# Optimization experiments

Hardware: AMD Instinct MI355X
Metric: run time of the kernel (lower is better)

## Reference

```python
import jax, jax.numpy as jnp
import numpy as np

B, O, D = 256, 128, 128          # batch, out_features (positions), per-position feat
IN = O * D                        # flattened in_features = 16384
NEG = -9.0e15                     # matches torch's -9e15 mask value


def setup_inputs() -> dict:
    key = jax.random.key(0)
    k1, k2 = jax.random.split(key, 2)
    enc = jax.random.normal(k1, (B, O, D), jnp.float32)
    W = jax.random.normal(k2, (O, IN), jnp.float32) / np.float32(np.sqrt(IN))
    b = jnp.zeros((O,), jnp.float32)
    return {"enc": enc, "W": W, "b": b}


def _step(enc, mask, W, b, k_count, key):
    """One decode step: linear -> error probe -> masked log-softmax -> sample.
    enc: [B,O,D], mask: [B,O] (1 = still available). k_count = #already-masked per row."""
    p = enc.reshape(B, IN) @ W.T + b                       # [B,O] raw scores
    order = jnp.argsort(-p, axis=1)                        # descending argsort of RAW p
    top_idx = jnp.take(order, k_count, axis=1)             # [B] (k_count+1)-th largest
    err = (jnp.take_along_axis(mask, top_idx[:, None], 1)[:, 0] == 0).astype(jnp.int32)
    pm = jnp.where(mask == 0, NEG, p)
    logp = jax.nn.log_softmax(pm, axis=1)                  # [B,O]
    pos = jax.random.categorical(key, logp)                # multinomial(exp(logp), 1)
    ls = jnp.take_along_axis(logp, pos[:, None], 1)[:, 0]  # chosen log-prob [B]
    new_mask = mask - jax.nn.one_hot(pos, O, dtype=mask.dtype)
    return pos, ls, err, new_mask


def reference(enc, W, b):
    mask0 = jnp.ones((B, O), jnp.float32)
    keys = jax.random.split(jax.random.key(42), O)
    # step 0: no enc masking, all-ones mask (k_count = 0)
    pos0, ls0, err0, mask = _step(enc, mask0, W, b, 0, keys[0])

    def body(carry, xs):
        enc_c, mask = carry
        j, key = xs
        enc_c = enc_c * mask[:, :, None]                   # zero out chosen positions
        pos, ls, err, mask = _step(enc_c, mask, W, b, j, key)
        return (enc_c, mask), (pos, ls, err)

    (_, _), (poss, lss, errs) = jax.lax.scan(
        body, (enc, mask), (jnp.arange(1, O), keys[1:]))
    # original prepends each new position: column 0 = last step sampled
    positions = jnp.flip(jnp.concatenate([pos0[None], poss], axis=0), axis=0).T  # [B,O]
    log_softmaxs = ls0 + lss.sum(axis=0)                   # [B]
    errors = err0 + errs.sum(axis=0)                       # [B] int32
    return positions, log_softmaxs, errors
```

## Files before the change

### kernel.cpp

```cpp
#include <hip/hip_runtime.h>
#include <stdint.h>

#define B_   256
#define O_   128
#define D_   128
#define IN_  16384
#define NEGF (-9.0e15f)
#define TINYF 1.1754943508222875e-38f

__device__ __forceinline__ void tf2x32(uint32_t k0, uint32_t k1,
                                       uint32_t x0, uint32_t x1,
                                       uint32_t* o0, uint32_t* o1) {
  uint32_t k2 = k0 ^ k1 ^ 0x1BD11BDAu;
#define TFR(r) { x0 += x1; x1 = (x1 << (r)) | (x1 >> (32 - (r))); x1 ^= x0; }
  x0 += k0; x1 += k1;
  TFR(13) TFR(15) TFR(26) TFR(6)
  x0 += k1; x1 += k2 + 1u;
  TFR(17) TFR(29) TFR(16) TFR(24)
  x0 += k2; x1 += k0 + 2u;
  TFR(13) TFR(15) TFR(26) TFR(6)
  x0 += k0; x1 += k1 + 3u;
  TFR(17) TFR(29) TFR(16) TFR(24)
  x0 += k1; x1 += k2 + 4u;
  TFR(13) TFR(15) TFR(26) TFR(6)
  x0 += k2; x1 += k0 + 5u;
#undef TFR
  *o0 = x0; *o1 = x1;
}

__device__ __forceinline__ float gumbel_bits(uint32_t bits) {
  float f = __uint_as_float((bits >> 9) | 0x3f800000u) - 1.0f;
  float u = fmaxf(TINYF, f + TINYF);
  return -logf(-logf(u));
}

__device__ __forceinline__ uint32_t mono32(float x) {
  int b = __float_as_int(x);
  return (uint32_t)b ^ ((uint32_t)(b >> 31) | 0x80000000u);
}

__device__ __forceinline__ float rl_f(float v, int l) {
  return __int_as_float(__builtin_amdgcn_readlane(__float_as_int(v), l));
}

#define DPPF(x, ctrl) __int_as_float(__builtin_amdgcn_mov_dpp( \
    __float_as_int(x), (ctrl), 0xf, 0xf, true))

__device__ __forceinline__ float wredmaxf(float x) {
  x = fmaxf(x, DPPF(x, 0xB1));
  x = fmaxf(x, DPPF(x, 0x4E));
  x = fmaxf(x, DPPF(x, 0x141));
  x = fmaxf(x, DPPF(x, 0x140));
  x = fmaxf(x, DPPF(x, 0x142));
  x = fmaxf(x, DPPF(x, 0x143));
  return rl_f(x, 63);
}
__device__ __forceinline__ float wredsumf(float x) {
  x = x + DPPF(x, 0xB1);
  x = x + DPPF(x, 0x4E);
  x = x + DPPF(x, 0x141);
  x = x + DPPF(x, 0x140);
  x = x + DPPF(x, 0x142);
  x = x + DPPF(x, 0x143);
  return rl_f(x, 63);
}

__global__ __launch_bounds__(256, 2) void build_M(
    const float* __restrict__ enc, const float* __restrict__ W,
    float* __restrict__ M) {
  const int p   = blockIdx.x;
  const int og0 = (blockIdx.y & 1) * 64;
  const int b0  = (blockIdx.y >> 1) * 128;
  const int t   = threadIdx.x;

  __shared__ float Ws[64 * 132];

  {
    const int rgrp = t >> 5;
    const int c16  = t & 31;
#pragma unroll
    for (int k = 0; k < 8; k++) {
      int row = k * 8 + rgrp;
      *(float4*)(Ws + row * 132 + c16 * 4) =
          *(const float4*)(W + (size_t)(og0 + row) * IN_ + p * D_ + c16 * 4);
    }
  }

  const int og = t & 15;
  const int bg = t >> 4;

  const float* eb = enc + ((size_t)(b0 + bg) * O_ + p) * D_;
  const size_t bstride = (size_t)16 * O_ * D_;

  float4 ev[8], evn[8];
#pragma unroll
  for (int bi = 0; bi < 8; bi++)
    ev[bi] = *(const float4*)(eb + bi * bstride);

  __syncthreads();

  float acc0[8][4] = {}, acc1[8][4] = {};

  for (int dc = 0; dc < 128; dc += 4) {
    if (dc < 124) {
#pragma unroll
      for (int bi = 0; bi < 8; bi++)
        evn[bi] = *(const float4*)(eb + bi * bstride + dc + 4);
    }
    float4 wv[4];
#pragma unroll
    for (int oi = 0; oi < 4; oi++)
      wv[oi] = *(const float4*)(Ws + (og + 16 * oi) * 132 + dc);
#pragma unroll
    for (int bi = 0; bi < 8; bi++)
#pragma unroll
      for (int oi = 0; oi < 4; oi++) {
        acc0[bi][oi] += ev[bi].x * wv[oi].x;
        acc1[bi][oi] += ev[bi].y * wv[oi].y;
        acc0[bi][oi] += ev[bi].z * wv[oi].z;
        acc1[bi][oi] += ev[bi].w * wv[oi].w;
      }
#pragma unroll
    for (int bi = 0; bi < 8; bi++) ev[bi] = evn[bi];
  }

#pragma unroll
  for (int bi = 0; bi < 8; bi++) {
    int b = b0 + bg + 16 * bi;
#pragma unroll
    for (int oi = 0; oi < 4; oi++) {
      int o = og0 + og + 16 * oi;
      M[((size_t)b * O_ + p) * O_ + o] = acc0[bi][oi] + acc1[bi][oi];
    }
  }
}

__global__ __launch_bounds__(512, 1) void sampler(
    const float* __restrict__ M, const float* __restrict__ bias,
    const float* __restrict__ enc, const float* __restrict__ W, int use_M,
    float* __restrict__ out_pos, float* __restrict__ out_ls,
    float* __restrict__ out_err) {
  const int b = blockIdx.x;
  const int t = threadIdx.x;
  const int lane = t & 63;
  const int w = t >> 6;

  __shared__ float  Mlds[O_ * O_];
  __shared__ float  Glds[O_ * O_];
  __shared__ double snapPd[16 * 64 * 2];
  __shared__ unsigned long long snapMk[16 * 2];
  __shared__ double lsSlot[16];
  __shared__ int    errSlot[16];
  __shared__ int    posb[O_];
  __shared__ int    flagG[16];
  __shared__ int    chainRel[16];
  __shared__ int    stageDone;

  volatile int* vFlagG = flagG;
  volatile int* vRel   = chainRel;
  volatile int* vSD    = &stageDone;

  const float b1f = bias[lane], b2f = bias[lane + 64];

  if (t < 16) { flagG[t] = 0; chainRel[t] = 0; }
  if (t == 16) stageDone = 0;
  __syncthreads();

  if (!use_M) {
    for (int idx = t; idx < O_ * O_; idx += 512) {
      int p = idx >> 7, o = idx & 127;
      const float* er = enc + ((size_t)b * O_ + p) * D_;
      const float* wr = W + (size_t)o * IN_ + p * D_;
      float s = 0.f;
      for (int d = 0; d < D_; d += 4) {
        float4 e4 = *(const float4*)(er + d);
        float4 w4 = *(const float4*)(wr + d);
        s += e4.x * w4.x + e4.y * w4.y + e4.z * w4.z + e4.w * w4.w;
      }
      Mlds[p * O_ + ((o & 63) << 1) + (o >> 6)] = s;
    }
    __syncthreads();
    if (t == 0) *vSD = 4;
  } else if (w < 4) {
    const float* Mb = M + (size_t)b * O_ * O_;
    for (int p = w * 32; p < w * 32 + 32; p++) {
      float v1 = Mb[p * O_ + lane];
      float v2 = Mb[p * O_ + 64 + lane];
      float2 mv; mv.x = v1; mv.y = v2;
      *(float2*)&Mlds[p * O_ + 2 * lane] = mv;
    }
    __threadfence_block();
    if (lane == 0) atomicAdd(&stageDone, 1);
  }

  if (w >= 4) {
#pragma unroll 1
    for (int k = 0; k < 4; k++) {
      int c = (w - 4) + 4 * k;
      for (int r = 8 * c; r < 8 * c + 8; r++) {
        uint32_t k0j, k1j, w0, w1;
        tf2x32(0u, 42u, 0u, (uint32_t)r, &k0j, &k1j);
        uint32_t m1 = (uint32_t)(b * O_ + lane);
        tf2x32(k0j, k1j, 0u, m1, &w0, &w1);
        float g1 = gumbel_bits(w0 ^ w1);
        tf2x32(k0j, k1j, 0u, m1 + 64u, &w0, &w1);
        float g2 = gumbel_bits(w0 ^ w1);
        float2 gv; gv.x = g1; gv.y = g2;
        *(float2*)&Glds[r * O_ + 2 * lane] = gv;
      }
      __threadfence_block();
      if (lane == 0) vFlagG[c] = 1;
    }
  }

  if (w == 0) {
    __builtin_amdgcn_s_setprio(3);
    while (*vSD < 4) __builtin_amdgcn_s_sleep(1);
    __threadfence_block();

    double Pd1 = 0.0, Pd2 = 0.0;
    for (int p = 0; p < O_; p++) {
      float2 mv = *(float2*)&Mlds[p * O_ + 2 * lane];
      Pd1 += (double)mv.x;
      Pd2 += (double)mv.y;
    }

    int mk1 = 0, mk2 = 0;
    unsigned long long bmk1 = 0ull, bmk2 = 0ull;
    while (vFlagG[0] == 0) __builtin_amdgcn_s_sleep(1);
    __threadfence_block();
    float2 gcur = *(float2*)&Glds[2 * lane];

    for (int j = 0; j < O_; j++) {
      if ((j & 7) == 0) {
        int c = j >> 3;
        if (c < 15) {
          while (vFlagG[c + 1] == 0) __builtin_amdgcn_s_sleep(1);
          __threadfence_block();
        }
        double2 pv; pv.x = Pd1; pv.y = Pd2;
        *(double2*)&snapPd[(c * 64 + lane) * 2] = pv;
        if (lane == 0) { snapMk[c * 2] = bmk1; snapMk[c * 2 + 1] = bmk2; }
      }
      float pm1 = mk1 ? NEGF : ((float)Pd1 + b1f);
      float pm2 = mk2 ? NEGF : ((float)Pd2 + b2f);
      float2 gnext;
      if (j < O_ - 1) gnext = *(float2*)&Glds[(j + 1) * O_ + 2 * lane];

      float z1 = pm1 + gcur.x, z2 = pm2 + gcur.y;
      float m = fmaxf(z1, z2);
      m = fmaxf(m, DPPF(m, 0xB1));
      m = fmaxf(m, DPPF(m, 0x4E));
      m = fmaxf(m, DPPF(m, 0x141));
      m = fmaxf(m, DPPF(m, 0x140));
      m = fmaxf(m, DPPF(m, 0x142));
      m = fmaxf(m, DPPF(m, 0x143));
      float zm = rl_f(m, 63);
      float thr = zm - 1e-2f;
      unsigned long long n1 = __ballot(z1 > thr);
      unsigned long long n2 = __ballot(z2 > thr);

      int pos;
      if (__popcll(n1) + __popcll(n2) == 1) {
        pos = n1 ? (__ffsll(n1) - 1) : (64 + __ffsll(n2) - 1);
      } else {
        float mx = wredmaxf(fmaxf(pm1, pm2));
        float s1 = pm1 - mx, s2 = pm2 - mx;
        float ss = wredsumf(expf(s1) + expf(s2));
        float lse = logf(ss);
        float y1 = (s1 - lse) + gcur.x;
        float y2 = (s2 - lse) + gcur.y;
        float ym = wredmaxf(fmaxf(y1, y2));
        unsigned long long c1 = __ballot(y1 == ym);
        unsigned long long c2 = __ballot(y2 == ym);
        pos = c1 ? (__ffsll(c1) - 1) : (64 + __ffsll(c2) - 1);
      }

      if (lane == 0) posb[j] = pos;
      mk1 |= (lane == pos);
      mk2 |= (lane + 64 == pos);
      if (pos < 64) bmk1 |= 1ull << pos; else bmk2 |= 1ull << (pos - 64);
      float2 mv = *(float2*)&Mlds[pos * O_ + 2 * lane];
      Pd1 -= (double)mv.x;
      Pd2 -= (double)mv.y;
      if ((j & 7) == 7) {
        __threadfence_block();
        if (lane == 0) vRel[j >> 3] = 1;
      }
      gcur = gnext;
    }
    out_pos[(size_t)b * O_ + lane]      = (float)posb[127 - lane];
    out_pos[(size_t)b * O_ + 64 + lane] = (float)posb[63 - lane];
  }

  if (w >= 1) {
    for (int c = w - 1; c < 16; c += 7) {
      while (vRel[c] == 0) __builtin_amdgcn_s_sleep(1);
      __threadfence_block();
      double2 pv = *(double2*)&snapPd[(c * 64 + lane) * 2];
      double P1 = pv.x, P2 = pv.y;
      unsigned long long bmk1 = snapMk[c * 2], bmk2 = snapMk[c * 2 + 1];
      double ls_acc = 0.0;
      int err_acc = 0;
      for (int j = 8 * c; j < 8 * c + 8; j++) {
        float p1 = (float)P1 + b1f;
        float p2 = (float)P2 + b2f;
        uint64_t K1 = ((uint64_t)mono32(p1) << 7) | (uint32_t)(127 - lane);
        uint64_t K2 = ((uint64_t)mono32(p2) << 7) | (uint32_t)(63 - lane);
        uint64_t P = 0;
#pragma unroll
        for (int bit = 38; bit >= 0; --bit) {
          uint64_t cand = P | (1ull << bit);
          int c1 = __popcll(__ballot(K1 >= cand));
          int c2 = __popcll(__ballot(K2 >= cand));
          if (c1 + c2 > j) P = cand;
        }
        unsigned long long t1 = __ballot(K1 == P), t2 = __ballot(K2 == P);
        int topl, msk;
        if (t1) { topl = __ffsll(t1) - 1; msk = (int)((bmk1 >> topl) & 1); }
        else    { topl = __ffsll(t2) - 1; msk = (int)((bmk2 >> topl) & 1); }
        err_acc += msk;

        float pm1 = ((bmk1 >> lane) & 1) ? NEGF : p1;
        float pm2 = ((bmk2 >> lane) & 1) ? NEGF : p2;
        float mx = wredmaxf(fmaxf(pm1, pm2));
        float ss = wredsumf(expf(pm1 - mx) + expf(pm2 - mx));
        float lse = logf(ss);
        int pos = posb[j];
        float psel = rl_f((pos < 64) ? p1 : p2, pos & 63);
        ls_acc += (double)((psel - mx) - lse);

        if (pos < 64) bmk1 |= 1ull << pos; else bmk2 |= 1ull << (pos - 64);
        float2 mv = *(float2*)&Mlds[pos * O_ + 2 * lane];
        P1 -= (double)mv.x;
        P2 -= (double)mv.y;
      }
      if (lane == 0) { lsSlot[c] = ls_acc; errSlot[c] = err_acc; }
    }
  }
  __syncthreads();

  if (t == 0) {
    double lt = 0.0; int et = 0;
    for (int i = 0; i < 16; i++) { lt += lsSlot[i]; et += errSlot[i]; }
    out_ls[b]  = (float)lt;
    out_err[b] = (float)et;
  }
}

extern "C" void kernel_launch(void* const* d_in, const int* in_sizes, int n_in,
                              void* d_out, int out_size, void* d_ws, size_t ws_size,
                              hipStream_t stream) {
  const float* enc  = (const float*)d_in[0];
  const float* W    = (const float*)d_in[1];
  const float* bias = (const float*)d_in[2];
  float* out     = (float*)d_out;
  float* out_pos = out;
  float* out_ls  = out + B_ * O_;
  float* out_err = out + B_ * O_ + B_;

  float* M = (float*)d_ws;
  const size_t needM = (size_t)B_ * O_ * O_ * sizeof(float);
  int use_M = (ws_size >= needM) ? 1 : 0;

  if (use_M) build_M<<<dim3(O_, 4), 256, 0, stream>>>(enc, W, M);
  sampler<<<dim3(B_), 512, 0, stream>>>(M, bias, enc, W, use_M,
                                        out_pos, out_ls, out_err);
}
```

Before: 150.7 us.

## Rebalance sampler warps: parallel column sums, shared key cache, split tail chunk

The column-sum prefix that wave 0 used to compute serially over all 128 rows is now split across waves 1-4 as partial double sums, and wave 0 only adds four partials. The per-row Threefry key derivation is computed once into shared memory, and Gumbel generation is spread over more waves, with waves 1-4 handling the later chunks. The final 8-step scoring chunk is split into two 4-step chunks so the tail work after the serial chain finishes is shorter. Bias plus Gumbel is also precomputed one step ahead to shorten the serial critical path. The cost is extra shared memory and more complex flag and chunk bookkeeping. Changing the order of the double summation can also change rounding slightly.

```diff
diff --git a/kernel.cpp b/kernel.cpp
--- a/kernel.cpp
+++ b/kernel.cpp
@@ -147,14 +147,16 @@
 
   __shared__ float  Mlds[O_ * O_];
   __shared__ float  Glds[O_ * O_];
-  __shared__ double snapPd[16 * 64 * 2];
-  __shared__ unsigned long long snapMk[16 * 2];
-  __shared__ double lsSlot[16];
-  __shared__ int    errSlot[16];
+  __shared__ double snapPd[17 * 64 * 2];
+  __shared__ unsigned long long snapMk[17 * 2];
+  __shared__ double lsSlot[17];
+  __shared__ int    errSlot[17];
   __shared__ int    posb[O_];
   __shared__ int    flagG[16];
-  __shared__ int    chainRel[16];
+  __shared__ int    chainRel[17];
   __shared__ int    stageDone;
+  __shared__ double partPd[4][64][2];
+  __shared__ uint32_t Klds[O_ * 2];
 
   volatile int* vFlagG = flagG;
   volatile int* vRel   = chainRel;
@@ -162,8 +164,13 @@
 
   const float b1f = bias[lane], b2f = bias[lane + 64];
 
-  if (t < 16) { flagG[t] = 0; chainRel[t] = 0; }
-  if (t == 16) stageDone = 0;
+  if (t < O_) {
+    uint32_t a, bb;
+    tf2x32(0u, 42u, 0u, (uint32_t)t, &a, &bb);
+    Klds[2 * t] = a; Klds[2 * t + 1] = bb;
+  }
+  if (t < 17) { chainRel[t] = 0; if (t < 16) flagG[t] = 0; }
+  if (t == 17) stageDone = 0;
   __syncthreads();
 
   if (!use_M) {
@@ -180,26 +187,41 @@
       Mlds[p * O_ + ((o & 63) << 1) + (o >> 6)] = s;
     }
     __syncthreads();
-    if (t == 0) *vSD = 4;
-  } else if (w < 4) {
+    if (w >= 1 && w <= 4) {
+      int q = w - 1;
+      double P1 = 0.0, P2 = 0.0;
+      for (int p = 32 * q; p < 32 * q + 32; p++) {
+        float2 mv = *(float2*)&Mlds[p * O_ + 2 * lane];
+        P1 += (double)mv.x;
+        P2 += (double)mv.y;
+      }
+      partPd[q][lane][0] = P1; partPd[q][lane][1] = P2;
+      __threadfence_block();
+      if (lane == 0) atomicAdd(&stageDone, 1);
+    }
+  } else if (w >= 1 && w <= 4) {
+    int q = w - 1;
     const float* Mb = M + (size_t)b * O_ * O_;
-    for (int p = w * 32; p < w * 32 + 32; p++) {
+    double P1 = 0.0, P2 = 0.0;
+    for (int p = 32 * q; p < 32 * q + 32; p++) {
       float v1 = Mb[p * O_ + lane];
       float v2 = Mb[p * O_ + 64 + lane];
       float2 mv; mv.x = v1; mv.y = v2;
       *(float2*)&Mlds[p * O_ + 2 * lane] = mv;
-    }
+      P1 += (double)v1;
+      P2 += (double)v2;
+    }
+    partPd[q][lane][0] = P1; partPd[q][lane][1] = P2;
     __threadfence_block();
     if (lane == 0) atomicAdd(&stageDone, 1);
   }
 
-  if (w >= 4) {
+  if (w >= 5) {
 #pragma unroll 1
-    for (int k = 0; k < 4; k++) {
-      int c = (w - 4) + 4 * k;
+    for (int c = w - 5; c < 8; c += 3) {
       for (int r = 8 * c; r < 8 * c + 8; r++) {
-        uint32_t k0j, k1j, w0, w1;
-        tf2x32(0u, 42u, 0u, (uint32_t)r, &k0j, &k1j);
+        uint32_t k0j = Klds[2 * r], k1j = Klds[2 * r + 1];
+        uint32_t w0, w1;
         uint32_t m1 = (uint32_t)(b * O_ + lane);
         tf2x32(k0j, k1j, 0u, m1, &w0, &w1);
         float g1 = gumbel_bits(w0 ^ w1);
@@ -211,6 +233,23 @@
       __threadfence_block();
       if (lane == 0) vFlagG[c] = 1;
     }
+  } else if (w >= 1) {
+#pragma unroll 1
+    for (int c = 7 + w; c < 16; c += 4) {
+      for (int r = 8 * c; r < 8 * c + 8; r++) {
+        uint32_t k0j = Klds[2 * r], k1j = Klds[2 * r + 1];
+        uint32_t w0, w1;
+        uint32_t m1 = (uint32_t)(b * O_ + lane);
+        tf2x32(k0j, k1j, 0u, m1, &w0, &w1);
+        float g1 = gumbel_bits(w0 ^ w1);
+        tf2x32(k0j, k1j, 0u, m1 + 64u, &w0, &w1);
+        float g2 = gumbel_bits(w0 ^ w1);
+        float2 gv; gv.x = g1; gv.y = g2;
+        *(float2*)&Glds[r * O_ + 2 * lane] = gv;
+      }
+      __threadfence_block();
+      if (lane == 0) vFlagG[c] = 1;
+    }
   }
 
   if (w == 0) {
@@ -218,36 +257,36 @@
     while (*vSD < 4) __builtin_amdgcn_s_sleep(1);
     __threadfence_block();
 
-    double Pd1 = 0.0, Pd2 = 0.0;
-    for (int p = 0; p < O_; p++) {
-      float2 mv = *(float2*)&Mlds[p * O_ + 2 * lane];
-      Pd1 += (double)mv.x;
-      Pd2 += (double)mv.y;
-    }
+    double Pd1 = ((partPd[0][lane][0] + partPd[1][lane][0]) +
+                  partPd[2][lane][0]) + partPd[3][lane][0];
+    double Pd2 = ((partPd[0][lane][1] + partPd[1][lane][1]) +
+                  partPd[2][lane][1]) + partPd[3][lane][1];
 
     int mk1 = 0, mk2 = 0;
     unsigned long long bmk1 = 0ull, bmk2 = 0ull;
     while (vFlagG[0] == 0) __builtin_amdgcn_s_sleep(1);
     __threadfence_block();
     float2 gcur = *(float2*)&Glds[2 * lane];
+    float bz1 = b1f + gcur.x, bz2 = b2f + gcur.y;
 
     for (int j = 0; j < O_; j++) {
-      if ((j & 7) == 0) {
+      if ((j & 7) == 0 || j == 124) {
         int c = j >> 3;
-        if (c < 15) {
+        if ((j & 7) == 0 && c < 15) {
           while (vFlagG[c + 1] == 0) __builtin_amdgcn_s_sleep(1);
           __threadfence_block();
         }
+        int sc = (j < 124) ? (j >> 3) : 16;
         double2 pv; pv.x = Pd1; pv.y = Pd2;
-        *(double2*)&snapPd[(c * 64 + lane) * 2] = pv;
-        if (lane == 0) { snapMk[c * 2] = bmk1; snapMk[c * 2 + 1] = bmk2; }
-      }
-      float pm1 = mk1 ? NEGF : ((float)Pd1 + b1f);
-      float pm2 = mk2 ? NEGF : ((float)Pd2 + b2f);
+        *(double2*)&snapPd[(sc * 64 + lane) * 2] = pv;
+        if (lane == 0) { snapMk[sc * 2] = bmk1; snapMk[sc * 2 + 1] = bmk2; }
+      }
+      float pmf1 = (float)Pd1, pmf2 = (float)Pd2;
+      float z1 = mk1 ? NEGF : (pmf1 + bz1);
+      float z2 = mk2 ? NEGF : (pmf2 + bz2);
       float2 gnext;
       if (j < O_ - 1) gnext = *(float2*)&Glds[(j + 1) * O_ + 2 * lane];
 
-      float z1 = pm1 + gcur.x, z2 = pm2 + gcur.y;
       float m = fmaxf(z1, z2);
       m = fmaxf(m, DPPF(m, 0xB1));
       m = fmaxf(m, DPPF(m, 0x4E));
@@ -264,6 +303,8 @@
       if (__popcll(n1) + __popcll(n2) == 1) {
         pos = n1 ? (__ffsll(n1) - 1) : (64 + __ffsll(n2) - 1);
       } else {
+        float pm1 = mk1 ? NEGF : (pmf1 + b1f);
+        float pm2 = mk2 ? NEGF : (pmf2 + b2f);
         float mx = wredmaxf(fmaxf(pm1, pm2));
         float s1 = pm1 - mx, s2 = pm2 - mx;
         float ss = wredsumf(expf(s1) + expf(s2));
@@ -283,18 +324,18 @@
       float2 mv = *(float2*)&Mlds[pos * O_ + 2 * lane];
       Pd1 -= (double)mv.x;
       Pd2 -= (double)mv.y;
-      if ((j & 7) == 7) {
-        __threadfence_block();
-        if (lane == 0) vRel[j >> 3] = 1;
-      }
+      if (j == 123) { __threadfence_block(); if (lane == 0) vRel[15] = 1; }
+      else if (j == 127) { __threadfence_block(); if (lane == 0) vRel[16] = 1; }
+      else if ((j & 7) == 7) { __threadfence_block(); if (lane == 0) vRel[j >> 3] = 1; }
       gcur = gnext;
+      bz1 = b1f + gcur.x; bz2 = b2f + gcur.y;
     }
     out_pos[(size_t)b * O_ + lane]      = (float)posb[127 - lane];
     out_pos[(size_t)b * O_ + 64 + lane] = (float)posb[63 - lane];
   }
 
   if (w >= 1) {
-    for (int c = w - 1; c < 16; c += 7) {
+    for (int c = w - 1; c < 17; c += 7) {
       while (vRel[c] == 0) __builtin_amdgcn_s_sleep(1);
       __threadfence_block();
       double2 pv = *(double2*)&snapPd[(c * 64 + lane) * 2];
@@ -302,7 +343,9 @@
       unsigned long long bmk1 = snapMk[c * 2], bmk2 = snapMk[c * 2 + 1];
       double ls_acc = 0.0;
       int err_acc = 0;
-      for (int j = 8 * c; j < 8 * c + 8; j++) {
+      int j0  = (c < 15) ? 8 * c : (120 + 4 * (c - 15));
+      int jend = (c < 15) ? (j0 + 8) : (j0 + 4);
+      for (int j = j0; j < jend; j++) {
         float p1 = (float)P1 + b1f;
         float p2 = (float)P2 + b2f;
         uint64_t K1 = ((uint64_t)mono32(p1) << 7) | (uint32_t)(127 - lane);
@@ -342,7 +385,7 @@
 
   if (t == 0) {
     double lt = 0.0; int et = 0;
-    for (int i = 0; i < 16; i++) { lt += lsSlot[i]; et += errSlot[i]; }
+    for (int i = 0; i < 17; i++) { lt += lsSlot[i]; et += errSlot[i]; }
     out_ls[b]  = (float)lt;
     out_err[b] = (float)et;
   }
```

Measured after the change: 156.8 us. 1.04x slower.

## Shorten sampler critical path: split tail chunks, parallel P init, speculative row load

Applied to the files above, without the earlier changes.

Several changes aim at the serial wave-0 sampling chain. Column sums of M are now computed in parallel by four waves and combined from partials, and the per-row Threefry keys are precomputed once into LDS. The first Gumbel rows are produced by all four generator waves so that sampling can start earlier. Inside the loop the M row for the argmax is loaded speculatively before the near-tie check, and z is computed one step ahead. The last chunk is also split into smaller pieces (4,2,2) so the trailing ls/err waves finish sooner. The cost is more LDS, extra snapshots and more complex flag logic, and the double summation order changes slightly.

```diff
diff --git a/kernel.cpp b/kernel.cpp
--- a/kernel.cpp
+++ b/kernel.cpp
@@ -147,14 +147,17 @@
 
   __shared__ float  Mlds[O_ * O_];
   __shared__ float  Glds[O_ * O_];
-  __shared__ double snapPd[16 * 64 * 2];
-  __shared__ unsigned long long snapMk[16 * 2];
-  __shared__ double lsSlot[16];
-  __shared__ int    errSlot[16];
+  __shared__ double snapPd[18 * 64 * 2];
+  __shared__ unsigned long long snapMk[18 * 2];
+  __shared__ double lsSlot[18];
+  __shared__ int    errSlot[18];
   __shared__ int    posb[O_];
   __shared__ int    flagG[16];
-  __shared__ int    chainRel[16];
+  __shared__ int    chainRel[18];
   __shared__ int    stageDone;
+  __shared__ int    g0cnt, g1cnt;
+  __shared__ double partPd[3][64][2];
+  __shared__ uint32_t Klds[O_ * 2];
 
   volatile int* vFlagG = flagG;
   volatile int* vRel   = chainRel;
@@ -162,10 +165,19 @@
 
   const float b1f = bias[lane], b2f = bias[lane + 64];
 
-  if (t < 16) { flagG[t] = 0; chainRel[t] = 0; }
-  if (t == 16) stageDone = 0;
+  if (t < O_) {
+    uint32_t a, bb;
+    tf2x32(0u, 42u, 0u, (uint32_t)t, &a, &bb);
+    Klds[2 * t] = a; Klds[2 * t + 1] = bb;
+  }
+  if (t < 16) flagG[t] = 0;
+  if (t >= 32 && t < 50) chainRel[t - 32] = 0;
+  if (t == 64) stageDone = 0;
+  if (t == 65) g0cnt = 0;
+  if (t == 66) g1cnt = 0;
   __syncthreads();
 
+  double pq1 = 0.0, pq2 = 0.0;
   if (!use_M) {
     for (int idx = t; idx < O_ * O_; idx += 512) {
       int p = idx >> 7, o = idx & 127;
@@ -180,56 +192,93 @@
       Mlds[p * O_ + ((o & 63) << 1) + (o >> 6)] = s;
     }
     __syncthreads();
-    if (t == 0) *vSD = 4;
+    if (w < 4) {
+      double P1 = 0.0, P2 = 0.0;
+      for (int p = 32 * w; p < 32 * w + 32; p++) {
+        float2 mv = *(float2*)&Mlds[p * O_ + 2 * lane];
+        P1 += (double)mv.x;
+        P2 += (double)mv.y;
+      }
+      if (w == 0) { pq1 = P1; pq2 = P2; }
+      else {
+        partPd[w - 1][lane][0] = P1; partPd[w - 1][lane][1] = P2;
+        __threadfence_block();
+        if (lane == 0) atomicAdd(&stageDone, 1);
+      }
+    }
   } else if (w < 4) {
     const float* Mb = M + (size_t)b * O_ * O_;
-    for (int p = w * 32; p < w * 32 + 32; p++) {
+    double P1 = 0.0, P2 = 0.0;
+    for (int p = 32 * w; p < 32 * w + 32; p++) {
       float v1 = Mb[p * O_ + lane];
       float v2 = Mb[p * O_ + 64 + lane];
       float2 mv; mv.x = v1; mv.y = v2;
       *(float2*)&Mlds[p * O_ + 2 * lane] = mv;
-    }
+      P1 += (double)v1;
+      P2 += (double)v2;
+    }
+    if (w == 0) { pq1 = P1; pq2 = P2; }
+    else {
+      partPd[w - 1][lane][0] = P1; partPd[w - 1][lane][1] = P2;
+      __threadfence_block();
+      if (lane == 0) atomicAdd(&stageDone, 1);
+    }
+  }
+
+#define GUMROW(r) {                                                    \
+    uint32_t k0j = Klds[2 * (r)], k1j = Klds[2 * (r) + 1];             \
+    uint32_t w0, w1;                                                   \
+    uint32_t m1 = (uint32_t)(b * O_ + lane);                           \
+    tf2x32(k0j, k1j, 0u, m1, &w0, &w1);                                \
+    float g1 = gumbel_bits(w0 ^ w1);                                   \
+    tf2x32(k0j, k1j, 0u, m1 + 64u, &w0, &w1);                          \
+    float g2 = gumbel_bits(w0 ^ w1);                                   \
+    float2 gv; gv.x = g1; gv.y = g2;                                   \
+    *(float2*)&Glds[(r) * O_ + 2 * lane] = gv;                         \
+  }
+
+  if (w >= 4) {
+    const int ww = w - 4;
+    GUMROW(2 * ww) GUMROW(2 * ww + 1)
     __threadfence_block();
-    if (lane == 0) atomicAdd(&stageDone, 1);
-  }
-
-  if (w >= 4) {
+    if (lane == 0) {
+      int old = atomicAdd(&g0cnt, 1);
+      if (old == 3) vFlagG[0] = 1;
+    }
+    GUMROW(8 + 2 * ww) GUMROW(9 + 2 * ww)
+    __threadfence_block();
+    if (lane == 0) {
+      int old = atomicAdd(&g1cnt, 1);
+      if (old == 3) vFlagG[1] = 1;
+    }
 #pragma unroll 1
-    for (int k = 0; k < 4; k++) {
-      int c = (w - 4) + 4 * k;
-      for (int r = 8 * c; r < 8 * c + 8; r++) {
-        uint32_t k0j, k1j, w0, w1;
-        tf2x32(0u, 42u, 0u, (uint32_t)r, &k0j, &k1j);
-        uint32_t m1 = (uint32_t)(b * O_ + lane);
-        tf2x32(k0j, k1j, 0u, m1, &w0, &w1);
-        float g1 = gumbel_bits(w0 ^ w1);
-        tf2x32(k0j, k1j, 0u, m1 + 64u, &w0, &w1);
-        float g2 = gumbel_bits(w0 ^ w1);
-        float2 gv; gv.x = g1; gv.y = g2;
-        *(float2*)&Glds[r * O_ + 2 * lane] = gv;
-      }
+    for (int c = 2 + ww; c < 16; c += 4) {
+      for (int r = 8 * c; r < 8 * c + 8; r++) GUMROW(r)
       __threadfence_block();
       if (lane == 0) vFlagG[c] = 1;
     }
   }
+#undef GUMROW
 
   if (w == 0) {
     __builtin_amdgcn_s_setprio(3);
-    while (*vSD < 4) __builtin_amdgcn_s_sleep(1);
+    while (*vSD < 3) __builtin_amdgcn_s_sleep(1);
     __threadfence_block();
 
-    double Pd1 = 0.0, Pd2 = 0.0;
-    for (int p = 0; p < O_; p++) {
-      float2 mv = *(float2*)&Mlds[p * O_ + 2 * lane];
-      Pd1 += (double)mv.x;
-      Pd2 += (double)mv.y;
-    }
+    double Pd1 = ((pq1 + partPd[0][lane][0]) + partPd[1][lane][0]) +
+                 partPd[2][lane][0];
+    double Pd2 = ((pq2 + partPd[0][lane][1]) + partPd[1][lane][1]) +
+                 partPd[2][lane][1];
 
     int mk1 = 0, mk2 = 0;
     unsigned long long bmk1 = 0ull, bmk2 = 0ull;
     while (vFlagG[0] == 0) __builtin_amdgcn_s_sleep(1);
     __threadfence_block();
     float2 gcur = *(float2*)&Glds[2 * lane];
+
+    float pmf1 = (float)Pd1, pmf2 = (float)Pd2;
+    float bz1 = b1f + gcur.x, bz2 = b2f + gcur.y;
+    float z1 = pmf1 + bz1, z2 = pmf2 + bz2;
 
     for (int j = 0; j < O_; j++) {
       if ((j & 7) == 0) {
@@ -241,13 +290,13 @@
         double2 pv; pv.x = Pd1; pv.y = Pd2;
         *(double2*)&snapPd[(c * 64 + lane) * 2] = pv;
         if (lane == 0) { snapMk[c * 2] = bmk1; snapMk[c * 2 + 1] = bmk2; }
-      }
-      float pm1 = mk1 ? NEGF : ((float)Pd1 + b1f);
-      float pm2 = mk2 ? NEGF : ((float)Pd2 + b2f);
-      float2 gnext;
-      if (j < O_ - 1) gnext = *(float2*)&Glds[(j + 1) * O_ + 2 * lane];
-
-      float z1 = pm1 + gcur.x, z2 = pm2 + gcur.y;
+      } else if (j == 124 || j == 126) {
+        int sc = (j == 124) ? 16 : 17;
+        double2 pv; pv.x = Pd1; pv.y = Pd2;
+        *(double2*)&snapPd[(sc * 64 + lane) * 2] = pv;
+        if (lane == 0) { snapMk[sc * 2] = bmk1; snapMk[sc * 2 + 1] = bmk2; }
+      }
+
       float m = fmaxf(z1, z2);
       m = fmaxf(m, DPPF(m, 0xB1));
       m = fmaxf(m, DPPF(m, 0x4E));
@@ -256,14 +305,21 @@
       m = fmaxf(m, DPPF(m, 0x142));
       m = fmaxf(m, DPPF(m, 0x143));
       float zm = rl_f(m, 63);
+
+      unsigned long long e1 = __ballot(z1 == zm);
+      unsigned long long e2 = __ballot(z2 == zm);
+      int pos = e1 ? (__ffsll(e1) - 1) : (64 + __ffsll(e2) - 1);
+      float2 mv = *(float2*)&Mlds[pos * O_ + 2 * lane];
+
       float thr = zm - 1e-2f;
       unsigned long long n1 = __ballot(z1 > thr);
       unsigned long long n2 = __ballot(z2 > thr);
-
-      int pos;
-      if (__popcll(n1) + __popcll(n2) == 1) {
-        pos = n1 ? (__ffsll(n1) - 1) : (64 + __ffsll(n2) - 1);
-      } else {
+      float2 gnext = gcur;
+      if (j < O_ - 1) gnext = *(float2*)&Glds[(j + 1) * O_ + 2 * lane];
+
+      if (__popcll(n1) + __popcll(n2) != 1) {
+        float pm1 = mk1 ? NEGF : (pmf1 + b1f);
+        float pm2 = mk2 ? NEGF : (pmf2 + b2f);
         float mx = wredmaxf(fmaxf(pm1, pm2));
         float s1 = pm1 - mx, s2 = pm2 - mx;
         float ss = wredsumf(expf(s1) + expf(s2));
@@ -274,27 +330,34 @@
         unsigned long long c1 = __ballot(y1 == ym);
         unsigned long long c2 = __ballot(y2 == ym);
         pos = c1 ? (__ffsll(c1) - 1) : (64 + __ffsll(c2) - 1);
+        mv = *(float2*)&Mlds[pos * O_ + 2 * lane];
       }
 
       if (lane == 0) posb[j] = pos;
       mk1 |= (lane == pos);
       mk2 |= (lane + 64 == pos);
       if (pos < 64) bmk1 |= 1ull << pos; else bmk2 |= 1ull << (pos - 64);
-      float2 mv = *(float2*)&Mlds[pos * O_ + 2 * lane];
       Pd1 -= (double)mv.x;
       Pd2 -= (double)mv.y;
-      if ((j & 7) == 7) {
-        __threadfence_block();
-        if (lane == 0) vRel[j >> 3] = 1;
-      }
+      pmf1 = (float)Pd1; pmf2 = (float)Pd2;
+
+      if (j < 120) {
+        if ((j & 7) == 7) { __threadfence_block(); if (lane == 0) vRel[j >> 3] = 1; }
+      } else if (j == 123) { __threadfence_block(); if (lane == 0) vRel[15] = 1; }
+      else if (j == 125) { __threadfence_block(); if (lane == 0) vRel[16] = 1; }
+      else if (j == 127) { __threadfence_block(); if (lane == 0) vRel[17] = 1; }
+
       gcur = gnext;
+      bz1 = b1f + gcur.x; bz2 = b2f + gcur.y;
+      z1 = mk1 ? NEGF : (pmf1 + bz1);
+      z2 = mk2 ? NEGF : (pmf2 + bz2);
     }
     out_pos[(size_t)b * O_ + lane]      = (float)posb[127 - lane];
     out_pos[(size_t)b * O_ + 64 + lane] = (float)posb[63 - lane];
   }
 
   if (w >= 1) {
-    for (int c = w - 1; c < 16; c += 7) {
+    for (int c = w - 1; c < 18; c += 7) {
       while (vRel[c] == 0) __builtin_amdgcn_s_sleep(1);
       __threadfence_block();
       double2 pv = *(double2*)&snapPd[(c * 64 + lane) * 2];
@@ -302,7 +365,9 @@
       unsigned long long bmk1 = snapMk[c * 2], bmk2 = snapMk[c * 2 + 1];
       double ls_acc = 0.0;
       int err_acc = 0;
-      for (int j = 8 * c; j < 8 * c + 8; j++) {
+      int j0   = (c < 15) ? 8 * c : ((c == 15) ? 120 : (124 + 2 * (c - 16)));
+      int jend = (c < 15) ? (j0 + 8) : ((c == 15) ? 124 : (j0 + 2));
+      for (int j = j0; j < jend; j++) {
         float p1 = (float)P1 + b1f;
         float p2 = (float)P2 + b2f;
         uint64_t K1 = ((uint64_t)mono32(p1) << 7) | (uint32_t)(127 - lane);
@@ -342,7 +407,7 @@
 
   if (t == 0) {
     double lt = 0.0; int et = 0;
-    for (int i = 0; i < 16; i++) { lt += lsSlot[i]; et += errSlot[i]; }
+    for (int i = 0; i < 18; i++) { lt += lsSlot[i]; et += errSlot[i]; }
     out_ls[b]  = (float)lt;
     out_err[b] = (float)et;
   }
```

Measured after the change: 148.0 us. About the same (-1.8%).
